# Kernel optimization log

Measured on AMD Instinct MI355X. Metric: run time of the kernel, lower is better.

Reference implementation:

```python
import jax, jax.numpy as jnp
import numpy as np

NUM_HEADS = 32
NUM_KV_GROUPS = 8
HEAD_DIM = 64  # dim_out // num_heads
DIM_IN = 2048
DIM_OUT = 2048


def setup_inputs() -> dict:
    key = jax.random.key(0)
    k_x, k_q, k_k, k_v, k_o = jax.random.split(key, 5)
    s = 0.02
    x = jax.random.normal(k_x, (1, 2048, DIM_IN), dtype=jnp.float32)
    wq = jax.random.normal(k_q, (DIM_IN, DIM_OUT), dtype=jnp.float32) * s
    wk = jax.random.normal(k_k, (DIM_IN, NUM_KV_GROUPS * HEAD_DIM), dtype=jnp.float32) * s
    wv = jax.random.normal(k_v, (DIM_IN, NUM_KV_GROUPS * HEAD_DIM), dtype=jnp.float32) * s
    wo = jax.random.normal(k_o, (DIM_OUT, DIM_OUT), dtype=jnp.float32) * s
    return {"x": x, "wq": wq, "wk": wk, "wv": wv, "wo": wo}


def reference(x, wq, wk, wv, wo):
    b, n, _ = x.shape
    g, r, d = NUM_KV_GROUPS, NUM_HEADS // NUM_KV_GROUPS, HEAD_DIM
    # projections
    q = (x @ wq).reshape(b, n, g, r, d)          # [b,n,g,r,d] heads grouped
    k = (x @ wk).reshape(b, n, g, d)             # [b,n,g,d]
    v = (x @ wv).reshape(b, n, g, d)
    # scores: repeat_interleave of K over group dim == broadcast over r
    scores = jnp.einsum('bqgrd,bkgd->bgrqk', q, k)  # [b,g,r,n,n]
    causal = jnp.tril(jnp.ones((n, n), dtype=bool))
    scores = jnp.where(causal, scores, -jnp.inf)
    attn = jax.nn.softmax(scores / jnp.sqrt(jnp.asarray(d, x.dtype)), axis=-1)
    ctx = jnp.einsum('bgrqk,bkgd->bqgrd', attn, v)  # [b,n,g,r,d]
    out = ctx.reshape(b, n, g * r * d) @ wo
    return out
```

## Files before the change

kernel.cpp:

```cpp
#include <hip/hip_runtime.h>


typedef __attribute__((ext_vector_type(8))) short bf16x8;
typedef __attribute__((ext_vector_type(4))) short bf16x4;
typedef __attribute__((ext_vector_type(4))) float f32x4;
typedef __attribute__((ext_vector_type(4))) unsigned u32x4;

__device__ __forceinline__ short f2bf(float f) {
  unsigned u = __builtin_bit_cast(unsigned, f);
  u += 0x7FFFu + ((u >> 16) & 1u);
  return (short)(u >> 16);
}

__device__ __forceinline__ unsigned pkbf(float a, float b) {
  const unsigned ua = __builtin_bit_cast(unsigned, a) + 0x8000u;
  const unsigned ub = __builtin_bit_cast(unsigned, b) + 0x8000u;
  return __builtin_amdgcn_perm(ub, ua, 0x07060302u);
}

__device__ __forceinline__ void pswap(unsigned a, unsigned b,
                                      unsigned& r0, unsigned& r1) {
  auto t = __builtin_amdgcn_permlane32_swap(a, b, false, false);
  auto u = __builtin_amdgcn_permlane16_swap(t[0], t[1], false, false);
  r0 = u[0]; r1 = u[1];
}

__device__ __forceinline__ void build_bfrag(const f32x4* sv, bf16x8& b0, bf16x8& b1) {
  const unsigned c0 = pkbf(sv[0][0], sv[0][1]), d0 = pkbf(sv[0][2], sv[0][3]);
  const unsigned c1 = pkbf(sv[1][0], sv[1][1]), d1 = pkbf(sv[1][2], sv[1][3]);
  const unsigned c2 = pkbf(sv[2][0], sv[2][1]), d2 = pkbf(sv[2][2], sv[2][3]);
  const unsigned c3 = pkbf(sv[3][0], sv[3][1]), d3 = pkbf(sv[3][2], sv[3][3]);
  unsigned q0, q1, q2, q3, r0, r1, r2, r3;
  pswap(c0, c1, q0, q2); pswap(d0, d1, q1, q3);
  pswap(c2, c3, r0, r2); pswap(d2, d3, r1, r3);
  b0 = __builtin_bit_cast(bf16x8, (u32x4){q0, q1, q2, q3});
  b1 = __builtin_bit_cast(bf16x8, (u32x4){r0, r1, r2, r3});
}

__device__ __forceinline__ void gload_lds16(const void* g, void* l) {
  __builtin_amdgcn_global_load_lds(
      (const __attribute__((address_space(1))) unsigned int*)g,
      (__attribute__((address_space(3))) unsigned int*)l, 16, 0, 0);
}

__global__ __launch_bounds__(256) void tcvt4(const float* __restrict__ wq,
                                             const float* __restrict__ wk,
                                             const float* __restrict__ wv,
                                             const float* __restrict__ wo,
                                             const float* __restrict__ x,
                                             short* __restrict__ dq,
                                             short* __restrict__ dk,
                                             short* __restrict__ dv,
                                             short* __restrict__ dwo,
                                             short* __restrict__ xb) {
  const int z = blockIdx.z;
  if (z == 4) {
    const int id = blockIdx.y * gridDim.x + blockIdx.x;
    const int i = (id * 256 + threadIdx.x) * 4;
    const float4 v = *(const float4*)&x[i];
    bf16x4 r;
    r[0] = f2bf(v.x); r[1] = f2bf(v.y); r[2] = f2bf(v.z); r[3] = f2bf(v.w);
    *(bf16x4*)&xb[i] = r;
    return;
  }
  const float* src;
  short* dst;
  int C;
  if (z == 0)      { src = wq; dst = dq;  C = 2048; }
  else if (z == 1) { src = wk; dst = dk;  C = 512; }
  else if (z == 2) { src = wv; dst = dv;  C = 512; }
  else             { src = wo; dst = dwo; C = 2048; }
  const int c0 = blockIdx.x * 32;
  if (c0 >= C) return;
  const int R = 2048;
  __shared__ float t[32][33];
  const int r0 = blockIdx.y * 32;
  const int tx = threadIdx.x & 31, ty = threadIdx.x >> 5;
#pragma unroll
  for (int i = 0; i < 4; ++i)
    t[ty + i * 8][tx] = src[(r0 + ty + i * 8) * C + c0 + tx];
  __syncthreads();
#pragma unroll
  for (int i = 0; i < 4; ++i)
    dst[(c0 + ty + i * 8) * R + r0 + tx] = f2bf(t[tx][ty + i * 8]);
}

template <int OUT_BF16, int BN, int FUSE_VT>
__global__ __launch_bounds__(128) void gemm_bt(const short* __restrict__ A,
                                               const short* __restrict__ B,
                                               void* __restrict__ Cv,
                                               int M, int N, int K,
                                               float cscale, int scale_cols,
                                               short* __restrict__ vt) {
  __shared__ short As[2][64 * 64];
  __shared__ short Bs[2][BN * 64];
  const int tid = threadIdx.x;
  const int lane = tid & 63, wid = tid >> 6;
  const int l15 = lane & 15, lg = lane >> 4;
  const int lr = lane >> 3, lc = lane & 7;
  const int nx = gridDim.x;
  const int orig = blockIdx.y * nx + blockIdx.x;
  const int nwg = nx * gridDim.y;
  const int wgid = (orig & 7) * (nwg >> 3) + (orig >> 3);
  const int bx = wgid % nx, by = wgid / nx;
  const int row0 = by * 64, col0 = bx * BN;
  const int sswz = l15 & 7;
  f32x4 acc[4][BN / 32] = {};
  const int arow = wid * 8 + lr;
  const short* ag = A + (row0 + arow) * K + (lc ^ lr) * 8;
  const short* bg = B + (col0 + arow) * K + (lc ^ lr) * 8;

  auto stage = [&](int b, int kk) {
    short* lA = &As[b][wid * 512];
    short* lB = &Bs[b][wid * 512];
#pragma unroll
    for (int c = 0; c < 4; ++c)
      gload_lds16(ag + c * 16 * K + kk, lA + c * 1024);
#pragma unroll
    for (int c = 0; c < BN / 16; ++c)
      gload_lds16(bg + c * 16 * K + kk, lB + c * 1024);
  };

  stage(0, 0);
  __syncthreads();
  const int nb = K / 64;
  int buf = 0;
  for (int t = 0; t < nb; ++t) {
    if (t + 1 < nb) stage(buf ^ 1, (t + 1) * 64);
#pragma unroll
    for (int x = 0; x < 2; ++x) {
      bf16x8 af[4], bfr[BN / 32];
#pragma unroll
      for (int m = 0; m < 4; ++m)
        af[m] = *(const bf16x8*)&As[buf][(m * 16 + l15) * 64 + (((x * 4 + lg) ^ sswz) * 8)];
#pragma unroll
      for (int n = 0; n < BN / 32; ++n)
        bfr[n] = *(const bf16x8*)&Bs[buf][(wid * (BN / 2) + n * 16 + l15) * 64 + (((x * 4 + lg) ^ sswz) * 8)];
#pragma unroll
      for (int m = 0; m < 4; ++m)
#pragma unroll
        for (int n = 0; n < BN / 32; ++n)
          acc[m][n] = __builtin_amdgcn_mfma_f32_16x16x32_bf16(af[m], bfr[n],
                                                              acc[m][n], 0, 0, 0);
    }
    __syncthreads();
    buf ^= 1;
  }
#pragma unroll
  for (int m = 0; m < 4; ++m)
#pragma unroll
    for (int n = 0; n < BN / 32; ++n)
#pragma unroll
      for (int i = 0; i < 4; ++i) {
        const int r = row0 + m * 16 + lg * 4 + i;
        const int c = col0 + wid * (BN / 2) + n * 16 + l15;
        float v = acc[m][n][i];
        if (c < scale_cols) v *= cscale;
        if (OUT_BF16)
          ((short*)Cv)[r * N + c] = f2bf(v);
        else
          ((float*)Cv)[r * N + c] = v;
        if (FUSE_VT && c >= 2560) vt[(c - 2560) * 2048 + r] = f2bf(v);
      }
}

__global__ __launch_bounds__(512) void attn_fwd(const short* __restrict__ QKV,
                                                const short* __restrict__ Vt,
                                                short* __restrict__ CTX) {
  const int ldq = 3072;
  const int hp = blockIdx.x;
  const int bxp = blockIdx.y;
  const int g = hp >> 1;
  const int h0 = g * 4 + (hp & 1) * 2;
  const int tid = threadIdx.x;
  const int lane = tid & 63, wid = tid >> 6;
  const int grp = wid >> 2;
  const int wq = wid & 3;
  const int l15 = lane & 15, lg = lane >> 4;

  __shared__ short Ks[2][2][64 * 64];
  __shared__ short Vs[2][2][64 * 64];
  __shared__ float CB[4][64][36];

  const int ltid = tid & 255;
  const int srow = ltid >> 3, sseg = ltid & 7;
  const int ssw = (sseg ^ (srow & 7)) * 8;
  const short* Kg = QKV + 2048 + g * 64 + sseg * 8;
  const short* Vg = Vt + (g * 64 + srow) * 2048 + sseg * 8;

  bf16x8 rk0, rk1, rv0, rv1;
  {
    const int tb = grp * 64;
    rk0 = *(const bf16x8*)&Kg[(tb + srow) * ldq];
    rk1 = *(const bf16x8*)&Kg[(tb + srow + 32) * ldq];
    rv0 = *(const bf16x8*)&Vg[tb];
    rv1 = *(const bf16x8*)&Vg[32 * 2048 + tb];
  }

#pragma unroll 1
  for (int half = 0; half < 2; ++half) {
    const int qb = half ? bxp : 31 - bxp;
    const int qrow0 = qb * 64 + wq * 16;

    bf16x8 qf[2][2];
#pragma unroll
    for (int hh = 0; hh < 2; ++hh)
#pragma unroll
      for (int kc = 0; kc < 2; ++kc)
        qf[hh][kc] = *(const bf16x8*)&QKV[(qrow0 + l15) * ldq + (h0 + hh) * 64 + kc * 32 + lg * 8];

    float l_run[2] = {0.f, 0.f};
    f32x4 accO[2][4] = {};

    const int nint = (qb >> 1) + 1;
#pragma unroll 1
    for (int j = 0; j < nint; ++j) {
      const int kt = 2 * j + grp;
      const bool valid = kt <= qb;
      const int buf = j & 1;
      if (valid) {
        *(bf16x8*)&Ks[grp][buf][srow * 64 + ssw] = rk0;
        *(bf16x8*)&Ks[grp][buf][(srow + 32) * 64 + ssw] = rk1;
        *(bf16x8*)&Vs[grp][buf][srow * 64 + ssw] = rv0;
        *(bf16x8*)&Vs[grp][buf][(srow + 32) * 64 + ssw] = rv1;
      }
      if (kt + 2 <= qb) {
        const int nb = (kt + 2) * 64;
        rk0 = *(const bf16x8*)&Kg[(nb + srow) * ldq];
        rk1 = *(const bf16x8*)&Kg[(nb + srow + 32) * ldq];
        rv0 = *(const bf16x8*)&Vg[nb];
        rv1 = *(const bf16x8*)&Vg[32 * 2048 + nb];
      }
      __syncthreads();
      if (!valid) continue;

      const int tokbase = kt * 64;
      f32x4 s[2][4];
      __builtin_amdgcn_s_setprio(1);
#pragma unroll
      for (int t = 0; t < 4; ++t) {
        s[0][t] = (f32x4){0.f, 0.f, 0.f, 0.f};
        s[1][t] = (f32x4){0.f, 0.f, 0.f, 0.f};
#pragma unroll
        for (int kc = 0; kc < 2; ++kc) {
          const bf16x8 kf =
              *(const bf16x8*)&Ks[grp][buf][(t * 16 + l15) * 64 + (((kc * 4 + lg) ^ (l15 & 7)) * 8)];
          s[0][t] = __builtin_amdgcn_mfma_f32_16x16x32_bf16(kf, qf[0][kc], s[0][t], 0, 0, 0);
          s[1][t] = __builtin_amdgcn_mfma_f32_16x16x32_bf16(kf, qf[1][kc], s[1][t], 0, 0, 0);
        }
      }
      __builtin_amdgcn_s_setprio(0);

      if (kt == qb) {
        const int kq = tokbase + lg * 4 - qrow0 - l15;
#pragma unroll
        for (int t = 0; t < 4; ++t)
#pragma unroll
          for (int i = 0; i < 4; ++i)
            if (kq + t * 16 + i > 0) { s[0][t][i] = -3e38f; s[1][t][i] = -3e38f; }
      }

#pragma unroll
      for (int hh = 0; hh < 2; ++hh) {
        float ts = 0.f;
#pragma unroll
        for (int t = 0; t < 4; ++t) {
          const float e0 = __builtin_amdgcn_exp2f(s[hh][t][0]);
          const float e1 = __builtin_amdgcn_exp2f(s[hh][t][1]);
          const float e2 = __builtin_amdgcn_exp2f(s[hh][t][2]);
          const float e3 = __builtin_amdgcn_exp2f(s[hh][t][3]);
          s[hh][t][0] = e0; s[hh][t][1] = e1; s[hh][t][2] = e2; s[hh][t][3] = e3;
          ts += (e0 + e1) + (e2 + e3);
        }
        ts += __shfl_xor(ts, 16);
        ts += __shfl_xor(ts, 32);
        l_run[hh] += ts;
      }

      bf16x8 pb[2][2];
      build_bfrag(s[0], pb[0][0], pb[0][1]);
      build_bfrag(s[1], pb[1][0], pb[1][1]);

      __builtin_amdgcn_s_setprio(1);
#pragma unroll
      for (int kc = 0; kc < 2; ++kc)
#pragma unroll
        for (int t2 = 0; t2 < 4; ++t2) {
          const bf16x8 vb =
              *(const bf16x8*)&Vs[grp][buf][(t2 * 16 + l15) * 64 + (((kc * 4 + lg) ^ (l15 & 7)) * 8)];
          accO[0][t2] = __builtin_amdgcn_mfma_f32_16x16x32_bf16(vb, pb[0][kc], accO[0][t2], 0, 0, 0);
          accO[1][t2] = __builtin_amdgcn_mfma_f32_16x16x32_bf16(vb, pb[1][kc], accO[1][t2], 0, 0, 0);
        }
      __builtin_amdgcn_s_setprio(0);
    }

    if (half == 0 && grp <= bxp) {
      const int tb = grp * 64;
      rk0 = *(const bf16x8*)&Kg[(tb + srow) * ldq];
      rk1 = *(const bf16x8*)&Kg[(tb + srow + 32) * ldq];
      rv0 = *(const bf16x8*)&Vg[tb];
      rv1 = *(const bf16x8*)&Vg[32 * 2048 + tb];
    }

    if (grp == 1) {
#pragma unroll
      for (int hh = 0; hh < 2; ++hh)
#pragma unroll
        for (int t2 = 0; t2 < 4; ++t2)
          *(f32x4*)&CB[wq][lane][hh * 16 + t2 * 4] = accO[hh][t2];
      *(float2*)&CB[wq][lane][32] = make_float2(l_run[0], l_run[1]);
    }
    __syncthreads();
    if (grp == 0) {
      const float2 lcb = *(const float2*)&CB[wq][lane][32];
#pragma unroll
      for (int hh = 0; hh < 2; ++hh) {
        const float lt = l_run[hh] + (hh ? lcb.y : lcb.x);
        const float inv = 1.0f / lt;
        f32x4 ov[4];
#pragma unroll
        for (int t2 = 0; t2 < 4; ++t2) {
          const f32x4 cb = *(const f32x4*)&CB[wq][lane][hh * 16 + t2 * 4];
#pragma unroll
          for (int i = 0; i < 4; ++i) ov[t2][i] = (accO[hh][t2][i] + cb[i]) * inv;
        }
        bf16x8 ob0, ob1;
        build_bfrag(ov, ob0, ob1);
        *(bf16x8*)&CTX[(qrow0 + l15) * 2048 + (h0 + hh) * 64 + lg * 8] = ob0;
        *(bf16x8*)&CTX[(qrow0 + l15) * 2048 + (h0 + hh) * 64 + 32 + lg * 8] = ob1;
      }
    }
  }
}

extern "C" void kernel_launch(void* const* d_in, const int* in_sizes, int n_in,
                              void* d_out, int out_size, void* d_ws, size_t ws_size,
                              hipStream_t stream) {
  (void)in_sizes; (void)n_in; (void)out_size; (void)ws_size;
  const float* x  = (const float*)d_in[0];
  const float* wq = (const float*)d_in[1];
  const float* wk = (const float*)d_in[2];
  const float* wv = (const float*)d_in[3];
  const float* wo = (const float*)d_in[4];
  float* out = (float*)d_out;

  char* ws = (char*)d_ws;
  short* Xb  = (short*)(ws);
  short* WT  = (short*)(ws + 8388608);
  short* WoT = (short*)(ws + 20971520);
  short* QKV = (short*)(ws + 29360128);
  short* Vt  = (short*)(ws + 41943040);
  short* CTX = (short*)(ws + 44040192);

  const float qscale = 0.125f * 1.4426950408889634f;

  { dim3 g(64, 64, 5);
    tcvt4<<<g, 256, 0, stream>>>(wq, wk, wv, wo, x,
                                 WT, WT + 2048 * 2048, WT + 2560 * 2048, WoT, Xb); }
  { dim3 g(32, 32);
    gemm_bt<1, 96, 1><<<g, 128, 0, stream>>>(Xb, WT, QKV, 2048, 3072, 2048,
                                             qscale, 2048, Vt); }
  { dim3 g(16, 16); attn_fwd<<<g, 512, 0, stream>>>(QKV, Vt, CTX); }
  { dim3 g(32, 32);
    gemm_bt<0, 64, 0><<<g, 128, 0, stream>>>(CTX, WoT, out, 2048, 2048, 2048,
                                             1.0f, 0, nullptr); }
}
```

Before: 122.3 us.

## Enlarge GEMM tiles to 128 rows with 4 waves and split V transpose

```diff
diff --git a/kernel.cpp b/kernel.cpp
--- a/kernel.cpp
+++ b/kernel.cpp
@@ -85,40 +85,55 @@
     dst[(c0 + ty + i * 8) * R + r0 + tx] = f2bf(t[tx][ty + i * 8]);
 }
 
-template <int OUT_BF16, int BN, int FUSE_VT>
-__global__ __launch_bounds__(128) void gemm_bt(const short* __restrict__ A,
+__global__ __launch_bounds__(256) void tbf(const short* __restrict__ src,
+                                           short* __restrict__ dst,
+                                           int R, int C, int ldsrc) {
+  __shared__ short t[32][33];
+  const int c0 = blockIdx.x * 32, r0 = blockIdx.y * 32;
+  const int tx = threadIdx.x & 31, ty = threadIdx.x >> 5;
+#pragma unroll
+  for (int i = 0; i < 4; ++i)
+    t[ty + i * 8][tx] = src[(r0 + ty + i * 8) * ldsrc + c0 + tx];
+  __syncthreads();
+#pragma unroll
+  for (int i = 0; i < 4; ++i)
+    dst[(c0 + ty + i * 8) * R + r0 + tx] = t[tx][ty + i * 8];
+}
+
+template <int OUT_BF16, int BN>
+__global__ __launch_bounds__(256) void gemm_bt(const short* __restrict__ A,
                                                const short* __restrict__ B,
                                                void* __restrict__ Cv,
                                                int M, int N, int K,
-                                               float cscale, int scale_cols,
-                                               short* __restrict__ vt) {
-  __shared__ short As[2][64 * 64];
+                                               float cscale, int scale_cols) {
+  constexpr int NF = BN / 32;
+  __shared__ short As[2][128 * 64];
   __shared__ short Bs[2][BN * 64];
   const int tid = threadIdx.x;
   const int lane = tid & 63, wid = tid >> 6;
   const int l15 = lane & 15, lg = lane >> 4;
-  const int lr = lane >> 3, lc = lane & 7;
+  const int lr8 = lane >> 3, lc8 = lane & 7;
+  const int wr = wid >> 1, wc = wid & 1;
   const int nx = gridDim.x;
   const int orig = blockIdx.y * nx + blockIdx.x;
   const int nwg = nx * gridDim.y;
   const int wgid = (orig & 7) * (nwg >> 3) + (orig >> 3);
   const int bx = wgid % nx, by = wgid / nx;
-  const int row0 = by * 64, col0 = bx * BN;
+  const int row0 = by * 128, col0 = bx * BN;
   const int sswz = l15 & 7;
-  f32x4 acc[4][BN / 32] = {};
-  const int arow = wid * 8 + lr;
-  const short* ag = A + (row0 + arow) * K + (lc ^ lr) * 8;
-  const short* bg = B + (col0 + arow) * K + (lc ^ lr) * 8;
+  f32x4 acc[4][NF] = {};
+  const short* ag = A + (row0 + wid * 32 + lr8) * K + (lc8 ^ lr8) * 8;
+  const short* bg = B + (col0 + wid * NF * 8 + lr8) * K + (lc8 ^ lr8) * 8;
 
   auto stage = [&](int b, int kk) {
-    short* lA = &As[b][wid * 512];
-    short* lB = &Bs[b][wid * 512];
+    short* lA = &As[b][wid * 2048];
+    short* lB = &Bs[b][wid * NF * 512];
 #pragma unroll
     for (int c = 0; c < 4; ++c)
-      gload_lds16(ag + c * 16 * K + kk, lA + c * 1024);
-#pragma unroll
-    for (int c = 0; c < BN / 16; ++c)
-      gload_lds16(bg + c * 16 * K + kk, lB + c * 1024);
+      gload_lds16(ag + c * 8 * K + kk, lA + c * 512);
+#pragma unroll
+    for (int c = 0; c < NF; ++c)
+      gload_lds16(bg + c * 8 * K + kk, lB + c * 512);
   };
 
   stage(0, 0);
@@ -129,17 +144,17 @@
     if (t + 1 < nb) stage(buf ^ 1, (t + 1) * 64);
 #pragma unroll
     for (int x = 0; x < 2; ++x) {
-      bf16x8 af[4], bfr[BN / 32];
+      bf16x8 af[4], bfr[NF];
 #pragma unroll
       for (int m = 0; m < 4; ++m)
-        af[m] = *(const bf16x8*)&As[buf][(m * 16 + l15) * 64 + (((x * 4 + lg) ^ sswz) * 8)];
-#pragma unroll
-      for (int n = 0; n < BN / 32; ++n)
-        bfr[n] = *(const bf16x8*)&Bs[buf][(wid * (BN / 2) + n * 16 + l15) * 64 + (((x * 4 + lg) ^ sswz) * 8)];
+        af[m] = *(const bf16x8*)&As[buf][(wr * 64 + m * 16 + l15) * 64 + (((x * 4 + lg) ^ sswz) * 8)];
+#pragma unroll
+      for (int n = 0; n < NF; ++n)
+        bfr[n] = *(const bf16x8*)&Bs[buf][(wc * (BN / 2) + n * 16 + l15) * 64 + (((x * 4 + lg) ^ sswz) * 8)];
 #pragma unroll
       for (int m = 0; m < 4; ++m)
 #pragma unroll
-        for (int n = 0; n < BN / 32; ++n)
+        for (int n = 0; n < NF; ++n)
           acc[m][n] = __builtin_amdgcn_mfma_f32_16x16x32_bf16(af[m], bfr[n],
                                                               acc[m][n], 0, 0, 0);
     }
@@ -149,18 +164,17 @@
 #pragma unroll
   for (int m = 0; m < 4; ++m)
 #pragma unroll
-    for (int n = 0; n < BN / 32; ++n)
+    for (int n = 0; n < NF; ++n)
 #pragma unroll
       for (int i = 0; i < 4; ++i) {
-        const int r = row0 + m * 16 + lg * 4 + i;
-        const int c = col0 + wid * (BN / 2) + n * 16 + l15;
+        const int r = row0 + wr * 64 + m * 16 + lg * 4 + i;
+        const int c = col0 + wc * (BN / 2) + n * 16 + l15;
         float v = acc[m][n][i];
         if (c < scale_cols) v *= cscale;
         if (OUT_BF16)
           ((short*)Cv)[r * N + c] = f2bf(v);
         else
           ((float*)Cv)[r * N + c] = v;
-        if (FUSE_VT && c >= 2560) vt[(c - 2560) * 2048 + r] = f2bf(v);
       }
 }
 
@@ -357,11 +371,12 @@
   { dim3 g(64, 64, 5);
     tcvt4<<<g, 256, 0, stream>>>(wq, wk, wv, wo, x,
                                  WT, WT + 2048 * 2048, WT + 2560 * 2048, WoT, Xb); }
-  { dim3 g(32, 32);
-    gemm_bt<1, 96, 1><<<g, 128, 0, stream>>>(Xb, WT, QKV, 2048, 3072, 2048,
-                                             qscale, 2048, Vt); }
+  { dim3 g(32, 16);
+    gemm_bt<1, 96><<<g, 256, 0, stream>>>(Xb, WT, QKV, 2048, 3072, 2048,
+                                          qscale, 2048); }
+  { dim3 g(16, 64); tbf<<<g, 256, 0, stream>>>(QKV + 2560, Vt, 2048, 512, 3072); }
   { dim3 g(16, 16); attn_fwd<<<g, 512, 0, stream>>>(QKV, Vt, CTX); }
-  { dim3 g(32, 32);
-    gemm_bt<0, 64, 0><<<g, 128, 0, stream>>>(CTX, WoT, out, 2048, 2048, 2048,
-                                             1.0f, 0, nullptr); }
-}
+  { dim3 g(32, 16);
+    gemm_bt<0, 64><<<g, 256, 0, stream>>>(CTX, WoT, out, 2048, 2048, 2048,
+                                          1.0f, 0); }
+}
```

After: 117.1 us. -4.2%, faster.
